# Kernel tuning notes

Measured on AMD Instinct MI355X. Metric: run time of the kernel, lower is better.

The kernel has to match this reference:

```python
import jax, jax.numpy as jnp
import numpy as np

D = 1024
H = 16

def setup_inputs() -> dict:
    key = jax.random.key(0)
    k1, k2, k3 = jax.random.split(key, 3)
    B, T = 4, 2048
    x = jax.random.normal(k1, (B, T, D), dtype=jnp.float32)
    # Linear weights stored as [in, out] so y = x @ W (equivalent to torch Linear with weight.T)
    W_attn = jax.random.normal(k2, (D, 3 * D), dtype=jnp.float32) * (1.0 / np.sqrt(D))
    W_proj = jax.random.normal(k3, (D, D), dtype=jnp.float32) * (1.0 / np.sqrt(D))
    return {"x": x, "W_attn": W_attn, "W_proj": W_proj}

def reference(x, W_attn, W_proj):
    B, T, _ = x.shape
    hd = D // H  # head dim
    qkv = x @ W_attn  # [B,T,3D]
    q, k, v = jnp.split(qkv, 3, axis=-1)
    # [B,T,D] -> [B,H,T,hd]
    q = q.reshape(B, T, H, hd).transpose(0, 2, 1, 3)
    k = k.reshape(B, T, H, hd).transpose(0, 2, 1, 3)
    v = v.reshape(B, T, H, hd).transpose(0, 2, 1, 3)
    scale = 1.0 / np.sqrt(hd).astype(np.float32)
    att = jnp.einsum('bhqd,bhkd->bhqk', q, k) * scale  # [B,H,T,T]
    causal = jnp.tril(jnp.ones((T, T), dtype=bool))
    att = jnp.where(causal[None, None], att, jnp.finfo(att.dtype).min)
    att = jax.nn.softmax(att, axis=-1)
    y = jnp.einsum('bhqk,bhkd->bhqd', att, v)  # [B,H,T,hd]
    y = y.transpose(0, 2, 1, 3).reshape(B, T, D)
    return y @ W_proj
```

## Files before the change

kernel.cpp:

```cpp
#include <hip/hip_runtime.h>


typedef __bf16 bf16;
typedef __attribute__((ext_vector_type(8))) __bf16 bf16x8;
typedef __attribute__((ext_vector_type(4))) __bf16 bf16x4;
typedef __attribute__((ext_vector_type(4))) float f4;

__device__ __forceinline__ void stage16(const bf16* g, bf16* l) {
    __builtin_amdgcn_global_load_lds((const __attribute__((address_space(1))) void*)g,
                                     (__attribute__((address_space(3))) void*)l,
                                     16, 0, 0);
}

__device__ __forceinline__ float fast_exp2(float x) {
    float r;
    asm("v_exp_f32 %0, %1" : "=v"(r) : "v"(x));
    return r;
}

__global__ __launch_bounds__(256)
void prep(const float* __restrict__ x, bf16* __restrict__ xb,
          const float* __restrict__ Wa, bf16* __restrict__ WtA,
          const float* __restrict__ Wp, bf16* __restrict__ WtP)
{
    __shared__ bf16 tile[64][65];
    int bid = blockIdx.x;
    int tid = threadIdx.x;
    if (bid < 8192) {
        int i = bid * 256 + tid;
        float4 v = ((const float4*)x)[i];
        bf16x4 o = { (bf16)v.x, (bf16)v.y, (bf16)v.z, (bf16)v.w };
        *(bf16x4*)&xb[i * 4] = o;
        return;
    }
    const float* src; bf16* dst; int R, C, c0, r0;
    if (bid < 8960) {
        int t = bid - 8192;
        src = Wa; dst = WtA; R = 1024; C = 3072;
        c0 = (t % 48) * 64; r0 = (t / 48) * 64;
    } else {
        int t = bid - 8960;
        src = Wp; dst = WtP; R = 1024; C = 1024;
        c0 = (t % 16) * 64; r0 = (t / 16) * 64;
    }
    for (int i = tid; i < 64 * 64; i += 256) {
        int r = i >> 6, c = i & 63;
        tile[r][c] = (bf16)src[(long)(r0 + r) * C + c0 + c];
    }
    __syncthreads();
    for (int i = tid; i < 64 * 64; i += 256) {
        int r = i >> 6, c = i & 63;
        dst[(long)(c0 + r) * R + r0 + c] = tile[c][r];
    }
}

#define VMW6 asm volatile("s_waitcnt vmcnt(6)" ::: "memory")
#define VMW0 asm volatile("s_waitcnt vmcnt(0)" ::: "memory")
#define CLOB asm volatile("" ::: "memory")
#define BARR __builtin_amdgcn_s_barrier()

template <typename OutT>
__global__ __launch_bounds__(512)
void gemm256(const bf16* __restrict__ A, const bf16* __restrict__ Bt,
             OutT* __restrict__ C, int lda, int ldb, int ldc, int K)
{
    extern __shared__ bf16 lds[];
    bf16* Asl = lds;
    bf16* Bsl = lds + 16384;
    int tid = threadIdx.x;
    int lane = tid & 63, wid = tid >> 6;
    int wm = wid >> 2, wn = wid & 3;
    int quad = lane >> 4, col = lane & 15;

    int nwg = gridDim.x * gridDim.y;
    int bid = blockIdx.y * gridDim.x + blockIdx.x;
    int swz = (bid & 7) * (nwg >> 3) + (bid >> 3);
    int bx = swz % gridDim.x, by = swz / gridDim.x;
    int m0 = by * 128, n0 = bx * 256;

    int NT = K >> 6;
    int srow = wid * 8 + (lane >> 3);
    int lincol = (lane & 7) * 8;
    int swcol  = ((lane & 7) ^ ((lane >> 3) & 7)) * 8;
    int xorv = (col & 7) << 4;
    int ke0 = ((quad * 16) ^ xorv) >> 1;
    int ke1 = ((quad * 16 + 64) ^ xorv) >> 1;

    f4 acc[4][4];
    #pragma unroll
    for (int mi = 0; mi < 4; ++mi)
        #pragma unroll
        for (int ni = 0; ni < 4; ++ni)
            acc[mi][ni] = (f4){0.f, 0.f, 0.f, 0.f};

    #define STG_HALF(mat, rb, ld, ts, dstb) do {                                \
        _Pragma("unroll")                                                       \
        for (int _i = 0; _i < 2; ++_i)                                          \
            stage16((mat) + (long)((rb) + _i * 64 + srow) * (ld) + (ts) * 64 + swcol, \
                    (dstb) + (_i * 64 + srow) * 64 + lincol);                   \
    } while (0)
    #define STGA(ts) STG_HALF(A, m0, lda, (ts), Asl + ((ts) & 1) * 8192)
    #define STGB(ts) do { bf16* _d = Bsl + ((ts) & 1) * 16384;                  \
        STG_HALF(Bt, n0,       ldb, (ts), _d);                                  \
        STG_HALF(Bt, n0 + 128, ldb, (ts), _d + 8192); } while (0)

    bf16x8 a[2][2], bb[4][2];
    #define RD_A(mp) do { _Pragma("unroll")                                     \
        for (int _m = 0; _m < 2; ++_m) {                                        \
            int _r = ab + ((mp) * 2 + _m) * 1024;                               \
            a[_m][0] = *(const bf16x8*)&Asl[_r + ke0];                          \
            a[_m][1] = *(const bf16x8*)&Asl[_r + ke1]; } } while (0)
    #define RD_B(np) do { _Pragma("unroll")                                     \
        for (int _n = 0; _n < 2; ++_n) {                                        \
            int _r = bbo + ((np) * 2 + _n) * 1024;                              \
            bb[(np)*2+_n][0] = *(const bf16x8*)&Bsl[_r + ke0];                  \
            bb[(np)*2+_n][1] = *(const bf16x8*)&Bsl[_r + ke1]; } } while (0)
    #define MM(mp, np) do { __builtin_amdgcn_s_setprio(1);                      \
        _Pragma("unroll")                                                       \
        for (int _m = 0; _m < 2; ++_m)                                          \
            _Pragma("unroll")                                                   \
            for (int _n = 0; _n < 2; ++_n)                                      \
                _Pragma("unroll")                                               \
                for (int kk = 0; kk < 2; ++kk)                                  \
                    acc[(mp)*2+_m][(np)*2+_n] =                                 \
                        __builtin_amdgcn_mfma_f32_16x16x32_bf16(                \
                            a[_m][kk], bb[(np)*2+_n][kk],                       \
                            acc[(mp)*2+_m][(np)*2+_n], 0, 0, 0);                \
        __builtin_amdgcn_s_setprio(0); } while (0)

    STGB(0); STGA(0); STGB(1); STGA(1);
    VMW6; CLOB; BARR; CLOB;

    for (int t = 0; t < NT; ++t) {
        int b = t & 1;
        int ab  = b * 8192  + (wm * 64 + col) * 64;
        int bbo = b * 16384 + (wn * 64 + col) * 64;
        RD_A(0); RD_B(0); RD_B(1);
        CLOB;
        MM(0, 0); MM(0, 1);
        CLOB; BARR; CLOB;
        RD_A(1);
        if (t + 2 < NT) STGB(t + 2);
        CLOB;
        MM(1, 1); MM(1, 0);
        if (t + 2 < NT) { STGA(t + 2); VMW6; }
        else if (t + 1 < NT) { VMW0; }
        CLOB; BARR;
    }
    #undef STG_HALF
    #undef STGA
    #undef STGB
    #undef RD_A
    #undef RD_B
    #undef MM

    #pragma unroll
    for (int mi = 0; mi < 4; ++mi) {
        int rbase = m0 + wm * 64 + mi * 16 + quad * 4;
        #pragma unroll
        for (int ni = 0; ni < 4; ++ni) {
            int cc = n0 + wn * 64 + ni * 16 + col;
            #pragma unroll
            for (int r = 0; r < 4; ++r)
                C[(long)(rbase + r) * ldc + cc] = (OutT)acc[mi][ni][r];
        }
    }
}

#define QS 72
#define C_SL 0.18033688011112042f

__device__ __forceinline__ int vsw(int d, int k) {
    return d * 64 + ((((k >> 3) ^ (d & 7) ^ ((d >> 3) & 7)) & 7) << 3) + (k & 7);
}

__global__ __launch_bounds__(256)
void attn_mfma(bf16* __restrict__ qkv)
{
    __shared__ bf16 Ks[64 * QS];
    __shared__ bf16 Vt[64 * 64];
    __shared__ bf16 Ps[4 * 32 * QS];
    const int T = 2048, D3 = 3072;
    int tid = threadIdx.x;
    int lane = tid & 63, wid = tid >> 6;
    int quad = lane >> 4, col = lane & 15;
    int bh = blockIdx.x & 63;
    int qt = 15 - (blockIdx.x >> 6);
    int b = bh >> 4, h = bh & 15;
    long base = (long)b * T * D3 + h * 64;
    int q0 = qt * 128;
    int nk = 2 * qt + 2;
    int srow = tid >> 2, dseg = (tid & 3) * 16;
    int kg4 = (tid >> 4) * 4, dg4 = (tid & 15) * 4;
    bf16* Pw = &Ps[wid * 32 * QS];

    bf16x8 aq[2][2];
    #pragma unroll
    for (int nt = 0; nt < 2; ++nt) {
        const bf16* gq = &qkv[base + (long)(q0 + wid * 32 + nt * 16 + col) * D3 + quad * 8];
        aq[nt][0] = *(const bf16x8*)gq;
        aq[nt][1] = *(const bf16x8*)(gq + 32);
    }
    bf16 one1 = (bf16)1.0f;
    bf16x8 bones = {one1, one1, one1, one1, one1, one1, one1, one1};

    f4 of[2][4], lac[2];
    #pragma unroll
    for (int mg = 0; mg < 2; ++mg) {
        lac[mg] = (f4){0.f, 0.f, 0.f, 0.f};
        #pragma unroll
        for (int n = 0; n < 4; ++n) of[mg][n] = (f4){0.f, 0.f, 0.f, 0.f};
    }

    const bf16* g0 = &qkv[base + (long)srow * D3 + 1024 + dseg];
    bf16x8 kr0 = *(const bf16x8*)g0;
    bf16x8 kr1 = *(const bf16x8*)(g0 + 8);
    const bf16* gV = &qkv[base + (long)kg4 * D3 + 2048 + dg4];
    bf16x4 vr[4];
    #pragma unroll
    for (int j = 0; j < 4; ++j) vr[j] = *(const bf16x4*)(gV + (long)j * D3);

    for (int kt = 0; kt < nk; ++kt) {
        __syncthreads();
        *(bf16x8*)&Ks[srow * QS + dseg]     = kr0;
        *(bf16x8*)&Ks[srow * QS + dseg + 8] = kr1;
        #pragma unroll
        for (int i = 0; i < 4; ++i) {
            bf16x4 c = { vr[0][i], vr[1][i], vr[2][i], vr[3][i] };
            *(bf16x4*)&Vt[vsw(dg4 + i, kg4)] = c;
        }
        if (kt + 1 < nk) {
            const bf16* gKn = &qkv[base + (long)((kt + 1) * 64 + srow) * D3 + 1024 + dseg];
            kr0 = *(const bf16x8*)gKn;
            kr1 = *(const bf16x8*)(gKn + 8);
            const bf16* gVn = &qkv[base + (long)((kt + 1) * 64 + kg4) * D3 + 2048 + dg4];
            #pragma unroll
            for (int j = 0; j < 4; ++j) vr[j] = *(const bf16x4*)(gVn + (long)j * D3);
        }
        __syncthreads();
        bool diag = (kt >= nk - 2);
        int k0 = kt * 64;
        #pragma unroll
        for (int mt = 0; mt < 4; ++mt) {
            bf16x8 ak0 = *(const bf16x8*)&Ks[(mt * 16 + col) * QS + quad * 8];
            bf16x8 ak1 = *(const bf16x8*)&Ks[(mt * 16 + col) * QS + 32 + quad * 8];
            #pragma unroll
            for (int nt = 0; nt < 2; ++nt) {
                f4 z = (f4){0.f, 0.f, 0.f, 0.f};
                __builtin_amdgcn_s_setprio(1);
                z = __builtin_amdgcn_mfma_f32_16x16x32_bf16(ak0, aq[nt][0], z, 0, 0, 0);
                f4 st = __builtin_amdgcn_mfma_f32_16x16x32_bf16(ak1, aq[nt][1], z, 0, 0, 0);
                __builtin_amdgcn_s_setprio(0);
                bf16x4 pk;
                if (diag) {
                    int qg = q0 + wid * 32 + nt * 16 + col;
                    #pragma unroll
                    for (int r = 0; r < 4; ++r) {
                        float arg = fmaf(st[r], C_SL, -16.f);
                        if ((k0 + mt * 16 + quad * 4 + r) > qg) arg = -1e30f;
                        pk[r] = (bf16)fast_exp2(arg);
                    }
                } else {
                    #pragma unroll
                    for (int r = 0; r < 4; ++r)
                        pk[r] = (bf16)fast_exp2(fmaf(st[r], C_SL, -16.f));
                }
                *(bf16x4*)&Pw[(nt * 16 + col) * QS + mt * 16 + quad * 4] = pk;
            }
        }
        bf16x8 ap[2][2];
        #pragma unroll
        for (int mg = 0; mg < 2; ++mg) {
            ap[mg][0] = *(const bf16x8*)&Pw[(mg * 16 + col) * QS + quad * 8];
            ap[mg][1] = *(const bf16x8*)&Pw[(mg * 16 + col) * QS + 32 + quad * 8];
        }
        #pragma unroll
        for (int nd = 0; nd < 4; ++nd) {
            bf16x8 bv0 = *(const bf16x8*)&Vt[vsw(nd * 16 + col, quad * 8)];
            bf16x8 bv1 = *(const bf16x8*)&Vt[vsw(nd * 16 + col, 32 + quad * 8)];
            __builtin_amdgcn_s_setprio(1);
            of[0][nd] = __builtin_amdgcn_mfma_f32_16x16x32_bf16(ap[0][0], bv0, of[0][nd], 0, 0, 0);
            of[0][nd] = __builtin_amdgcn_mfma_f32_16x16x32_bf16(ap[0][1], bv1, of[0][nd], 0, 0, 0);
            of[1][nd] = __builtin_amdgcn_mfma_f32_16x16x32_bf16(ap[1][0], bv0, of[1][nd], 0, 0, 0);
            of[1][nd] = __builtin_amdgcn_mfma_f32_16x16x32_bf16(ap[1][1], bv1, of[1][nd], 0, 0, 0);
            __builtin_amdgcn_s_setprio(0);
        }
        __builtin_amdgcn_s_setprio(1);
        #pragma unroll
        for (int mg = 0; mg < 2; ++mg) {
            lac[mg] = __builtin_amdgcn_mfma_f32_16x16x32_bf16(ap[mg][0], bones, lac[mg], 0, 0, 0);
            lac[mg] = __builtin_amdgcn_mfma_f32_16x16x32_bf16(ap[mg][1], bones, lac[mg], 0, 0, 0);
        }
        __builtin_amdgcn_s_setprio(0);
    }
    #pragma unroll
    for (int mg = 0; mg < 2; ++mg)
        #pragma unroll
        for (int r = 0; r < 4; ++r) {
            float inv = 1.f / lac[mg][r];
            long yoff = base + (long)(q0 + wid * 32 + mg * 16 + quad * 4 + r) * D3;
            #pragma unroll
            for (int nd = 0; nd < 4; ++nd)
                qkv[yoff + nd * 16 + col] = (bf16)(of[mg][nd][r] * inv);
        }
}

extern "C" void kernel_launch(void* const* d_in, const int* in_sizes, int n_in,
                              void* d_out, int out_size, void* d_ws, size_t ws_size,
                              hipStream_t stream) {
    const float* x      = (const float*)d_in[0];
    const float* W_attn = (const float*)d_in[1];
    const float* W_proj = (const float*)d_in[2];
    float* out = (float*)d_out;

    bf16* qkv = (bf16*)d_ws;
    bf16* WtA = qkv + (size_t)8192 * 3072;
    bf16* WtP = WtA + (size_t)3072 * 1024;
    bf16* xb = (bf16*)d_out;

    static bool attr_set = false;
    if (!attr_set) {
        hipFuncSetAttribute((const void*)gemm256<bf16>,
                            hipFuncAttributeMaxDynamicSharedMemorySize, 98304);
        hipFuncSetAttribute((const void*)gemm256<float>,
                            hipFuncAttributeMaxDynamicSharedMemorySize, 98304);
        attr_set = true;
    }

    prep<<<9216, 256, 0, stream>>>(x, xb, W_attn, WtA, W_proj, WtP);
    gemm256<bf16><<<dim3(12, 64), 512, 98304, stream>>>(xb, WtA, qkv,
                                                        1024, 1024, 3072, 1024);
    attn_mfma<<<1024, 256, 0, stream>>>(qkv);
    gemm256<float><<<dim3(4, 64), 512, 98304, stream>>>(qkv, WtP, out,
                                                        3072, 1024, 1024, 1024);
}
```

Baseline: 239.5 us.

## Pair complementary causal query tiles per block for balanced attention work

Each attention block now handles two 64-row query tiles, one from the end of the sequence and its mirror from the start (31-g and g), so every block processes the same number of key/value tiles under the causal mask. Each wave covers 16 query rows instead of 32, which halves the P scratch buffer in LDS, and the per-tile QK/softmax/PV body is moved into a shared helper. The first pass prefetches the first K/V tile for the second pass. The aim is to remove the tail imbalance from blocks of very different lengths. In exchange, each loaded K/V tile feeds half as many query rows, so K/V global and LDS traffic roughly doubles.

```diff
diff --git a/kernel.cpp b/kernel.cpp
--- a/kernel.cpp
+++ b/kernel.cpp
@@ -174,53 +174,99 @@
     return d * 64 + ((((k >> 3) ^ (d & 7) ^ ((d >> 3) & 7)) & 7) << 3) + (k & 7);
 }
 
+__device__ __forceinline__ void attn_tile(
+    const bf16x8 (&aq)[2], f4 (&of)[4], f4 &lac, const bf16x8 &bones,
+    bf16* Pw, const bf16* Ks, const bf16* Vt,
+    int quad, int col, int qg, int k0, bool diag)
+{
+    #pragma unroll
+    for (int mt = 0; mt < 4; ++mt) {
+        bf16x8 ak0 = *(const bf16x8*)&Ks[(mt * 16 + col) * QS + quad * 8];
+        bf16x8 ak1 = *(const bf16x8*)&Ks[(mt * 16 + col) * QS + 32 + quad * 8];
+        f4 z = (f4){0.f, 0.f, 0.f, 0.f};
+        __builtin_amdgcn_s_setprio(1);
+        z = __builtin_amdgcn_mfma_f32_16x16x32_bf16(ak0, aq[0], z, 0, 0, 0);
+        f4 st = __builtin_amdgcn_mfma_f32_16x16x32_bf16(ak1, aq[1], z, 0, 0, 0);
+        __builtin_amdgcn_s_setprio(0);
+        bf16x4 pk;
+        if (diag) {
+            #pragma unroll
+            for (int r = 0; r < 4; ++r) {
+                float arg = fmaf(st[r], C_SL, -16.f);
+                if ((k0 + mt * 16 + quad * 4 + r) > qg) arg = -1e30f;
+                pk[r] = (bf16)fast_exp2(arg);
+            }
+        } else {
+            #pragma unroll
+            for (int r = 0; r < 4; ++r)
+                pk[r] = (bf16)fast_exp2(fmaf(st[r], C_SL, -16.f));
+        }
+        *(bf16x4*)&Pw[col * QS + mt * 16 + quad * 4] = pk;
+    }
+    bf16x8 ap0 = *(const bf16x8*)&Pw[col * QS + quad * 8];
+    bf16x8 ap1 = *(const bf16x8*)&Pw[col * QS + 32 + quad * 8];
+    #pragma unroll
+    for (int nd = 0; nd < 4; ++nd) {
+        bf16x8 bv0 = *(const bf16x8*)&Vt[vsw(nd * 16 + col, quad * 8)];
+        bf16x8 bv1 = *(const bf16x8*)&Vt[vsw(nd * 16 + col, 32 + quad * 8)];
+        __builtin_amdgcn_s_setprio(1);
+        of[nd] = __builtin_amdgcn_mfma_f32_16x16x32_bf16(ap0, bv0, of[nd], 0, 0, 0);
+        of[nd] = __builtin_amdgcn_mfma_f32_16x16x32_bf16(ap1, bv1, of[nd], 0, 0, 0);
+        __builtin_amdgcn_s_setprio(0);
+    }
+    __builtin_amdgcn_s_setprio(1);
+    lac = __builtin_amdgcn_mfma_f32_16x16x32_bf16(ap0, bones, lac, 0, 0, 0);
+    lac = __builtin_amdgcn_mfma_f32_16x16x32_bf16(ap1, bones, lac, 0, 0, 0);
+    __builtin_amdgcn_s_setprio(0);
+}
+
 __global__ __launch_bounds__(256)
 void attn_mfma(bf16* __restrict__ qkv)
 {
     __shared__ bf16 Ks[64 * QS];
     __shared__ bf16 Vt[64 * 64];
-    __shared__ bf16 Ps[4 * 32 * QS];
+    __shared__ bf16 Ps[4 * 16 * QS];
     const int T = 2048, D3 = 3072;
     int tid = threadIdx.x;
     int lane = tid & 63, wid = tid >> 6;
     int quad = lane >> 4, col = lane & 15;
     int bh = blockIdx.x & 63;
-    int qt = 15 - (blockIdx.x >> 6);
+    int g  = blockIdx.x >> 6;
     int b = bh >> 4, h = bh & 15;
     long base = (long)b * T * D3 + h * 64;
-    int q0 = qt * 128;
-    int nk = 2 * qt + 2;
+    int jA = 31 - g, jB = g;
+    int nkA = jA + 1, nkB = jB + 1;
     int srow = tid >> 2, dseg = (tid & 3) * 16;
     int kg4 = (tid >> 4) * 4, dg4 = (tid & 15) * 4;
-    bf16* Pw = &Ps[wid * 32 * QS];
-
-    bf16x8 aq[2][2];
-    #pragma unroll
-    for (int nt = 0; nt < 2; ++nt) {
-        const bf16* gq = &qkv[base + (long)(q0 + wid * 32 + nt * 16 + col) * D3 + quad * 8];
-        aq[nt][0] = *(const bf16x8*)gq;
-        aq[nt][1] = *(const bf16x8*)(gq + 32);
+    bf16* Pw = &Ps[wid * 16 * QS];
+    int q0wA = jA * 64 + wid * 16, q0wB = jB * 64 + wid * 16;
+
+    bf16x8 aqA[2], aqB[2];
+    {
+        const bf16* gq = &qkv[base + (long)(q0wA + col) * D3 + quad * 8];
+        aqA[0] = *(const bf16x8*)gq;
+        aqA[1] = *(const bf16x8*)(gq + 32);
+        const bf16* gq2 = &qkv[base + (long)(q0wB + col) * D3 + quad * 8];
+        aqB[0] = *(const bf16x8*)gq2;
+        aqB[1] = *(const bf16x8*)(gq2 + 32);
     }
     bf16 one1 = (bf16)1.0f;
     bf16x8 bones = {one1, one1, one1, one1, one1, one1, one1, one1};
 
-    f4 of[2][4], lac[2];
-    #pragma unroll
-    for (int mg = 0; mg < 2; ++mg) {
-        lac[mg] = (f4){0.f, 0.f, 0.f, 0.f};
-        #pragma unroll
-        for (int n = 0; n < 4; ++n) of[mg][n] = (f4){0.f, 0.f, 0.f, 0.f};
-    }
-
-    const bf16* g0 = &qkv[base + (long)srow * D3 + 1024 + dseg];
-    bf16x8 kr0 = *(const bf16x8*)g0;
-    bf16x8 kr1 = *(const bf16x8*)(g0 + 8);
+    f4 of[4], lac;
+    #pragma unroll
+    for (int n = 0; n < 4; ++n) of[n] = (f4){0.f, 0.f, 0.f, 0.f};
+    lac = (f4){0.f, 0.f, 0.f, 0.f};
+
+    const bf16* gK = &qkv[base + (long)srow * D3 + 1024 + dseg];
+    bf16x8 kr0 = *(const bf16x8*)gK;
+    bf16x8 kr1 = *(const bf16x8*)(gK + 8);
     const bf16* gV = &qkv[base + (long)kg4 * D3 + 2048 + dg4];
     bf16x4 vr[4];
     #pragma unroll
     for (int j = 0; j < 4; ++j) vr[j] = *(const bf16x4*)(gV + (long)j * D3);
 
-    for (int kt = 0; kt < nk; ++kt) {
+    for (int kt = 0; kt < nkA; ++kt) {
         __syncthreads();
         *(bf16x8*)&Ks[srow * QS + dseg]     = kr0;
         *(bf16x8*)&Ks[srow * QS + dseg + 8] = kr1;
@@ -229,7 +275,41 @@
             bf16x4 c = { vr[0][i], vr[1][i], vr[2][i], vr[3][i] };
             *(bf16x4*)&Vt[vsw(dg4 + i, kg4)] = c;
         }
-        if (kt + 1 < nk) {
+        {
+            int nxt = (kt + 1 < nkA) ? kt + 1 : 0;
+            const bf16* gKn = &qkv[base + (long)(nxt * 64 + srow) * D3 + 1024 + dseg];
+            kr0 = *(const bf16x8*)gKn;
+            kr1 = *(const bf16x8*)(gKn + 8);
+            const bf16* gVn = &qkv[base + (long)(nxt * 64 + kg4) * D3 + 2048 + dg4];
+            #pragma unroll
+            for (int j = 0; j < 4; ++j) vr[j] = *(const bf16x4*)(gVn + (long)j * D3);
+        }
+        __syncthreads();
+        attn_tile(aqA, of, lac, bones, Pw, Ks, Vt, quad, col,
+                  q0wA + col, kt * 64, kt == nkA - 1);
+    }
+    #pragma unroll
+    for (int r = 0; r < 4; ++r) {
+        float inv = 1.f / lac[r];
+        long yoff = base + (long)(q0wA + quad * 4 + r) * D3;
+        #pragma unroll
+        for (int nd = 0; nd < 4; ++nd)
+            qkv[yoff + nd * 16 + col] = (bf16)(of[nd][r] * inv);
+    }
+    #pragma unroll
+    for (int n = 0; n < 4; ++n) of[n] = (f4){0.f, 0.f, 0.f, 0.f};
+    lac = (f4){0.f, 0.f, 0.f, 0.f};
+
+    for (int kt = 0; kt < nkB; ++kt) {
+        __syncthreads();
+        *(bf16x8*)&Ks[srow * QS + dseg]     = kr0;
+        *(bf16x8*)&Ks[srow * QS + dseg + 8] = kr1;
+        #pragma unroll
+        for (int i = 0; i < 4; ++i) {
+            bf16x4 c = { vr[0][i], vr[1][i], vr[2][i], vr[3][i] };
+            *(bf16x4*)&Vt[vsw(dg4 + i, kg4)] = c;
+        }
+        if (kt + 1 < nkB) {
             const bf16* gKn = &qkv[base + (long)((kt + 1) * 64 + srow) * D3 + 1024 + dseg];
             kr0 = *(const bf16x8*)gKn;
             kr1 = *(const bf16x8*)(gKn + 8);
@@ -238,71 +318,17 @@
             for (int j = 0; j < 4; ++j) vr[j] = *(const bf16x4*)(gVn + (long)j * D3);
         }
         __syncthreads();
-        bool diag = (kt >= nk - 2);
-        int k0 = kt * 64;
-        #pragma unroll
-        for (int mt = 0; mt < 4; ++mt) {
-            bf16x8 ak0 = *(const bf16x8*)&Ks[(mt * 16 + col) * QS + quad * 8];
-            bf16x8 ak1 = *(const bf16x8*)&Ks[(mt * 16 + col) * QS + 32 + quad * 8];
-            #pragma unroll
-            for (int nt = 0; nt < 2; ++nt) {
-                f4 z = (f4){0.f, 0.f, 0.f, 0.f};
-                __builtin_amdgcn_s_setprio(1);
-                z = __builtin_amdgcn_mfma_f32_16x16x32_bf16(ak0, aq[nt][0], z, 0, 0, 0);
-                f4 st = __builtin_amdgcn_mfma_f32_16x16x32_bf16(ak1, aq[nt][1], z, 0, 0, 0);
-                __builtin_amdgcn_s_setprio(0);
-                bf16x4 pk;
-                if (diag) {
-                    int qg = q0 + wid * 32 + nt * 16 + col;
-                    #pragma unroll
-                    for (int r = 0; r < 4; ++r) {
-                        float arg = fmaf(st[r], C_SL, -16.f);
-                        if ((k0 + mt * 16 + quad * 4 + r) > qg) arg = -1e30f;
-                        pk[r] = (bf16)fast_exp2(arg);
-                    }
-                } else {
-                    #pragma unroll
-                    for (int r = 0; r < 4; ++r)
-                        pk[r] = (bf16)fast_exp2(fmaf(st[r], C_SL, -16.f));
-                }
-                *(bf16x4*)&Pw[(nt * 16 + col) * QS + mt * 16 + quad * 4] = pk;
-            }
-        }
-        bf16x8 ap[2][2];
-        #pragma unroll
-        for (int mg = 0; mg < 2; ++mg) {
-            ap[mg][0] = *(const bf16x8*)&Pw[(mg * 16 + col) * QS + quad * 8];
-            ap[mg][1] = *(const bf16x8*)&Pw[(mg * 16 + col) * QS + 32 + quad * 8];
-        }
-        #pragma unroll
-        for (int nd = 0; nd < 4; ++nd) {
-            bf16x8 bv0 = *(const bf16x8*)&Vt[vsw(nd * 16 + col, quad * 8)];
-            bf16x8 bv1 = *(const bf16x8*)&Vt[vsw(nd * 16 + col, 32 + quad * 8)];
-            __builtin_amdgcn_s_setprio(1);
-            of[0][nd] = __builtin_amdgcn_mfma_f32_16x16x32_bf16(ap[0][0], bv0, of[0][nd], 0, 0, 0);
-            of[0][nd] = __builtin_amdgcn_mfma_f32_16x16x32_bf16(ap[0][1], bv1, of[0][nd], 0, 0, 0);
-            of[1][nd] = __builtin_amdgcn_mfma_f32_16x16x32_bf16(ap[1][0], bv0, of[1][nd], 0, 0, 0);
-            of[1][nd] = __builtin_amdgcn_mfma_f32_16x16x32_bf16(ap[1][1], bv1, of[1][nd], 0, 0, 0);
-            __builtin_amdgcn_s_setprio(0);
-        }
-        __builtin_amdgcn_s_setprio(1);
-        #pragma unroll
-        for (int mg = 0; mg < 2; ++mg) {
-            lac[mg] = __builtin_amdgcn_mfma_f32_16x16x32_bf16(ap[mg][0], bones, lac[mg], 0, 0, 0);
-            lac[mg] = __builtin_amdgcn_mfma_f32_16x16x32_bf16(ap[mg][1], bones, lac[mg], 0, 0, 0);
-        }
-        __builtin_amdgcn_s_setprio(0);
-    }
-    #pragma unroll
-    for (int mg = 0; mg < 2; ++mg)
-        #pragma unroll
-        for (int r = 0; r < 4; ++r) {
-            float inv = 1.f / lac[mg][r];
-            long yoff = base + (long)(q0 + wid * 32 + mg * 16 + quad * 4 + r) * D3;
-            #pragma unroll
-            for (int nd = 0; nd < 4; ++nd)
-                qkv[yoff + nd * 16 + col] = (bf16)(of[mg][nd][r] * inv);
-        }
+        attn_tile(aqB, of, lac, bones, Pw, Ks, Vt, quad, col,
+                  q0wB + col, kt * 64, kt == nkB - 1);
+    }
+    #pragma unroll
+    for (int r = 0; r < 4; ++r) {
+        float inv = 1.f / lac[r];
+        long yoff = base + (long)(q0wB + quad * 4 + r) * D3;
+        #pragma unroll
+        for (int nd = 0; nd < 4; ++nd)
+            qkv[yoff + nd * 16 + col] = (bf16)(of[nd][r] * inv);
+    }
 }
 
 extern "C" void kernel_launch(void* const* d_in, const int* in_sizes, int n_in,
```

After: 253.7 us. 1.06x slower.

## Use 256x256 square-tile GEMM kernel for QKV projection

Applied to the files above, without the earlier changes.

Adds a new GEMM kernel with a 256x256 output tile (previous one was 128-row by 256-col) for the QKV projection. Each block loads A and B halves in a ping-pong, double-buffered LDS schedule of 128KB and interleaves quarter-tile MFMA groups with async global-to-LDS loads and barriers. The larger tile raises arithmetic intensity and halves the grid to 384 blocks, which cuts global/L2 traffic. In exchange it uses more LDS and registers per block and leaves fewer blocks to fill the 256 CUs.

```diff
diff --git a/kernel.cpp b/kernel.cpp
--- a/kernel.cpp
+++ b/kernel.cpp
@@ -58,6 +58,122 @@
 #define VMW0 asm volatile("s_waitcnt vmcnt(0)" ::: "memory")
 #define CLOB asm volatile("" ::: "memory")
 #define BARR __builtin_amdgcn_s_barrier()
+
+__global__ __launch_bounds__(512)
+void gemm256sq(const bf16* __restrict__ A, const bf16* __restrict__ Bt,
+               bf16* __restrict__ C, int lda, int ldb, int ldc, int K)
+{
+    extern __shared__ bf16 lds[];
+    bf16* Asl = lds;
+    bf16* Bsl = lds + 32768;
+    int tid = threadIdx.x;
+    int lane = tid & 63, wid = tid >> 6;
+    int wm = wid >> 2, wn = wid & 3;
+    int quad = lane >> 4, col = lane & 15;
+
+    int nwg = gridDim.x * gridDim.y;
+    int bid = blockIdx.y * gridDim.x + blockIdx.x;
+    int swz = (bid & 7) * (nwg >> 3) + (bid >> 3);
+    int bx = swz % gridDim.x, by = swz / gridDim.x;
+    int m0 = by * 256, n0 = bx * 256;
+
+    int NT = K >> 6;
+    int srow = wid * 8 + (lane >> 3);
+    int lincol = (lane & 7) * 8;
+    int swcol  = ((lane & 7) ^ ((lane >> 3) & 7)) * 8;
+    int xorv = (col & 7) << 4;
+    int ke0 = ((quad * 16) ^ xorv) >> 1;
+    int ke1 = ((quad * 16 + 64) ^ xorv) >> 1;
+
+    f4 acc[8][4];
+    #pragma unroll
+    for (int mi = 0; mi < 8; ++mi)
+        #pragma unroll
+        for (int ni = 0; ni < 4; ++ni)
+            acc[mi][ni] = (f4){0.f, 0.f, 0.f, 0.f};
+
+    #define STGH(mat, rb, ld, base0, h, ts) do { if ((ts) < NT) {               \
+        bf16* _d = (base0) + (((ts) & 1) * 2 + (h)) * 8192;                     \
+        _Pragma("unroll")                                                       \
+        for (int _i = 0; _i < 2; ++_i)                                          \
+            stage16((mat) + (long)((rb) + (h) * 128 + _i * 64 + srow) * (ld) + (ts) * 64 + swcol, \
+                    _d + (_i * 64 + srow) * 64 + lincol); } } while (0)
+    #define SA(h, ts) STGH(A,  m0, lda, Asl, h, ts)
+    #define SB(h, ts) STGH(Bt, n0, ldb, Bsl, h, ts)
+
+    bf16x8 a[4][2], b0[2][2], b1[2][2];
+    #define RDA(qm, bo) do { _Pragma("unroll")                                  \
+        for (int _m = 0; _m < 4; ++_m) {                                        \
+            int _r = (bo) + ((wm * 128 + (qm) * 64 + _m * 16 + col) << 6);      \
+            a[_m][0] = *(const bf16x8*)&Asl[_r + ke0];                          \
+            a[_m][1] = *(const bf16x8*)&Asl[_r + ke1]; } } while (0)
+    #define RDB(arr, qn, bo) do { _Pragma("unroll")                             \
+        for (int _n = 0; _n < 2; ++_n) {                                        \
+            int _r = (bo) + ((wn * 64 + (qn) * 32 + _n * 16 + col) << 6);       \
+            arr[_n][0] = *(const bf16x8*)&Bsl[_r + ke0];                        \
+            arr[_n][1] = *(const bf16x8*)&Bsl[_r + ke1]; } } while (0)
+    #define MMQ(qm, arr, qn) do { __builtin_amdgcn_s_setprio(1);                \
+        _Pragma("unroll")                                                       \
+        for (int _m = 0; _m < 4; ++_m)                                          \
+            _Pragma("unroll")                                                   \
+            for (int _n = 0; _n < 2; ++_n)                                      \
+                _Pragma("unroll")                                               \
+                for (int kk = 0; kk < 2; ++kk)                                  \
+                    acc[(qm)*4+_m][(qn)*2+_n] =                                 \
+                        __builtin_amdgcn_mfma_f32_16x16x32_bf16(                \
+                            a[_m][kk], arr[_n][kk],                             \
+                            acc[(qm)*4+_m][(qn)*2+_n], 0, 0, 0);                \
+        __builtin_amdgcn_s_setprio(0); } while (0)
+
+    SB(0, 0); SA(0, 0); SB(1, 0); SA(1, 0); SB(0, 1); SA(0, 1); SB(1, 1);
+    VMW6; CLOB; BARR; CLOB;
+
+    for (int t = 0; t < NT; t += 2) {
+        bool deep = (t + 3 < NT);
+        RDA(0, 0); RDB(b0, 0, 0);
+        SA(1, t + 1);
+        CLOB; BARR; CLOB; MMQ(0, b0, 0); CLOB; BARR;
+        RDB(b1, 1, 0);
+        SB(0, t + 2);
+        CLOB; BARR; CLOB; MMQ(0, b1, 1); CLOB; BARR;
+        RDA(1, 0);
+        SB(1, t + 2);
+        CLOB; BARR; CLOB; MMQ(1, b1, 1); CLOB; BARR;
+        SA(0, t + 2);
+        if (deep) { VMW6; } else { VMW0; }
+        CLOB; BARR; CLOB; MMQ(1, b0, 0); CLOB; BARR;
+        RDA(0, 16384); RDB(b0, 0, 16384);
+        SA(1, t + 2);
+        CLOB; BARR; CLOB; MMQ(0, b0, 0); CLOB; BARR;
+        RDB(b1, 1, 16384);
+        SB(0, t + 3);
+        CLOB; BARR; CLOB; MMQ(0, b1, 1); CLOB; BARR;
+        RDA(1, 16384);
+        SB(1, t + 3);
+        CLOB; BARR; CLOB; MMQ(1, b1, 1); CLOB; BARR;
+        SA(0, t + 3);
+        if (deep) { VMW6; } else { VMW0; }
+        CLOB; BARR; CLOB; MMQ(1, b0, 0); CLOB; BARR;
+    }
+    #undef STGH
+    #undef SA
+    #undef SB
+    #undef RDA
+    #undef RDB
+    #undef MMQ
+
+    #pragma unroll
+    for (int j = 0; j < 8; ++j) {
+        int rbase = m0 + wm * 128 + (j >> 2) * 64 + (j & 3) * 16 + quad * 4;
+        #pragma unroll
+        for (int n = 0; n < 4; ++n) {
+            int cc = n0 + wn * 64 + (n >> 1) * 32 + (n & 1) * 16 + col;
+            #pragma unroll
+            for (int r = 0; r < 4; ++r)
+                C[(long)(rbase + r) * ldc + cc] = (bf16)acc[j][n][r];
+        }
+    }
+}
 
 template <typename OutT>
 __global__ __launch_bounds__(512)
@@ -320,16 +436,16 @@
 
     static bool attr_set = false;
     if (!attr_set) {
-        hipFuncSetAttribute((const void*)gemm256<bf16>,
-                            hipFuncAttributeMaxDynamicSharedMemorySize, 98304);
+        hipFuncSetAttribute((const void*)gemm256sq,
+                            hipFuncAttributeMaxDynamicSharedMemorySize, 131072);
         hipFuncSetAttribute((const void*)gemm256<float>,
                             hipFuncAttributeMaxDynamicSharedMemorySize, 98304);
         attr_set = true;
     }
 
     prep<<<9216, 256, 0, stream>>>(x, xb, W_attn, WtA, W_proj, WtP);
-    gemm256<bf16><<<dim3(12, 64), 512, 98304, stream>>>(xb, WtA, qkv,
-                                                        1024, 1024, 3072, 1024);
+    gemm256sq<<<dim3(12, 32), 512, 131072, stream>>>(xb, WtA, qkv,
+                                                     1024, 1024, 3072, 1024);
     attn_mfma<<<1024, 256, 0, stream>>>(qkv);
     gemm256<float><<<dim3(4, 64), 512, 98304, stream>>>(qkv, WtP, out,
                                                         3072, 1024, 1024, 1024);
```

After: 236.7 us. No clear change (-1.2%).
